# Kernel optimization log

Measured on AMD Instinct MI355X. Metric: run time of the kernel, lower is better.

Reference implementation:

```python
import jax, jax.numpy as jnp
import numpy as np

HEAD_DIM = 64
EPS = 1e-06


def yat_dense(x, kernel, bias):
    # YatDense (nmn): y = (x.W)^2 / (||x - w||^2 + eps) * alpha_scale + b
    dot = x @ kernel                                  # [..., F]
    x_sq = jnp.sum(x * x, axis=-1, keepdims=True)     # [..., 1]
    w_sq = jnp.sum(kernel * kernel, axis=0)           # [F]
    dist = x_sq + w_sq - 2.0 * dot                    # squared euclidean distance
    y = (dot * dot) / (dist + EPS)
    feats = kernel.shape[1]
    scale = np.sqrt(feats) / np.log1p(feats)          # alpha=1 scaling
    return y * jnp.asarray(scale, x.dtype) + bias


def apply_rope(q, k):
    # q,k: [B,H,T,D]; interleaved-pair rotation, base 10000 (dim=HEAD_DIM)
    B, H, T, D = q.shape
    half = D // 2
    pos = jnp.arange(T, dtype=jnp.float32)
    freqs = 10000.0 ** (-jnp.arange(half, dtype=jnp.float32) / half)
    ang = pos[:, None] * freqs[None, :]               # [T, half]
    sin = jnp.sin(ang)[None, None, :, :, None]        # [1,1,T,half,1]
    cos = jnp.cos(ang)[None, None, :, :, None]

    def rot(t):
        ts = t.reshape(B, H, T, half, 2)
        t0, t1 = ts[..., 0:1], ts[..., 1:2]
        out = jnp.concatenate([t0 * cos - t1 * sin, t1 * cos + t0 * sin], axis=-1)
        return out.reshape(B, H, T, D)

    return rot(q), rot(k)


def setup_inputs() -> dict:
    key = jax.random.key(0)
    B, T, C, H = 2, 2048, 1024, 16
    k1, k2, k3, k4, k5 = jax.random.split(key, 5)
    x = jax.random.normal(k1, (B, T, C), dtype=jnp.float32)
    # causal mask, broadcast over batch
    mask = jnp.broadcast_to(jnp.tril(jnp.ones((T, T), dtype=bool))[None], (B, T, T))
    s = 1.0 / np.sqrt(C)
    w_attn = jax.random.normal(k2, (C, 3 * C), dtype=jnp.float32) * s
    b_attn = jnp.zeros((3 * C,), dtype=jnp.float32)
    w_proj = jax.random.normal(k3, (C, C), dtype=jnp.float32) * s
    b_proj = jnp.zeros((C,), dtype=jnp.float32)
    return {"x": x, "mask": mask, "w_attn": w_attn, "b_attn": b_attn,
            "w_proj": w_proj, "b_proj": b_proj}


def reference(x, mask, w_attn, b_attn, w_proj, b_proj):
    B, T, C = x.shape
    H = C // HEAD_DIM
    qkv = yat_dense(x, w_attn, b_attn)                     # [B,T,3C]
    qkv = qkv.reshape(B, T, 3, H, HEAD_DIM)
    q, k, v = jnp.moveaxis(qkv, 2, 0)                      # each [B,T,H,hd]
    q = jnp.swapaxes(q, 1, 2)                              # [B,H,T,hd]
    k = jnp.swapaxes(k, 1, 2)
    v = jnp.swapaxes(v, 1, 2)
    q, k = apply_rope(q, k)
    scale = jnp.asarray(np.sqrt(HEAD_DIM), x.dtype)
    attn = jnp.einsum('bhqd,bhkd->bhqk', q, k) / scale     # [B,H,T,T]
    neg = jnp.finfo(x.dtype).min
    attn = jnp.where(mask[:, None, :, :], attn, neg)
    attn = jax.nn.softmax(attn, axis=-1)
    out = jnp.einsum('bhqk,bhkd->bhqd', attn, v)           # [B,H,T,hd]
    out = jnp.swapaxes(out, 1, 2).reshape(B, T, C)
    return yat_dense(out, w_proj, b_proj)
```

## Files before the change

kernel.cpp:

```cpp
#include <hip/hip_runtime.h>
#include <hip/hip_bf16.h>
#include <cmath>

#define BB 2
#define TT 2048
#define CC 1024
#define HH 16
#define DD 64
#define ROWS (BB*TT)
#define N1 (3*CC)
#define EPS 1e-6f

using short8 = __attribute__((ext_vector_type(8))) short;
using f32x4  = __attribute__((ext_vector_type(4))) float;

__device__ __forceinline__ void gl_lds16(const __hip_bfloat16* g, unsigned short* l) {
    __builtin_amdgcn_global_load_lds(
        (const __attribute__((address_space(1))) unsigned int*)(g),
        (__attribute__((address_space(3))) unsigned int*)(l), 16, 0, 0);
}

__device__ __forceinline__ unsigned int bf16pair(float a, float b) {
    __hip_bfloat16 ha = (__hip_bfloat16)a, hb = (__hip_bfloat16)b;
    unsigned short ua = *(unsigned short*)&ha, ub = *(unsigned short*)&hb;
    return (unsigned int)ua | ((unsigned int)ub << 16);
}

__device__ __forceinline__ float bf2f(unsigned short u) {
    unsigned int v = (unsigned int)u << 16;
    return *(float*)&v;
}

__global__ void aux_rowsq(const float* __restrict__ X, float* __restrict__ xsq,
                          __hip_bfloat16* __restrict__ Xb, float* __restrict__ osq,
                          float* __restrict__ rope,
                          float* __restrict__ wsqa, float* __restrict__ wsqp) {
    int blk = blockIdx.x;
    int t = threadIdx.x;
    if (blk >= ROWS) {
        int idx = (blk - ROWS) * 256 + t;
        if (idx < N1) wsqa[idx] = 0.f;
        if (idx < CC) wsqp[idx] = 0.f;
        if (idx < TT * 32) {
            int tt = idx >> 5, i = idx & 31;
            double freq = pow(10000.0, -(double)i / 32.0);
            float ang = (float)tt * (float)freq;
            rope[idx * 2 + 0] = cosf(ang);
            rope[idx * 2 + 1] = sinf(ang);
        }
        return;
    }
    int row = blk;
    const float* xr = X + (size_t)row * CC;
    __hip_bfloat16* br = Xb + (size_t)row * CC;
    float p = 0.f;
#pragma unroll
    for (int i = 0; i < 4; ++i) {
        float v = xr[t + i * 256];
        p += v * v;
        br[t + i * 256] = (__hip_bfloat16)v;
    }
#pragma unroll
    for (int off = 32; off > 0; off >>= 1) p += __shfl_xor(p, off, 64);
    __shared__ float s4[4];
    if ((t & 63) == 0) s4[t >> 6] = p;
    __syncthreads();
    if (t == 0) { xsq[row] = s4[0] + s4[1] + s4[2] + s4[3]; osq[row] = 0.f; }
}

__global__ void transpose2(const float* __restrict__ Wa, __hip_bfloat16* __restrict__ WaT,
                           float* __restrict__ wsqa,
                           const float* __restrict__ Wp, __hip_bfloat16* __restrict__ WpT,
                           float* __restrict__ wsqp) {
    const float* W; __hip_bfloat16* Wt; float* wsq; int N;
    if (blockIdx.z == 0) { W = Wa; Wt = WaT; wsq = wsqa; N = N1; }
    else { if (blockIdx.x >= 16) return; W = Wp; Wt = WpT; wsq = wsqp; N = CC; }
    const int K = CC;
    __shared__ unsigned short tile[64][65];
    int n0 = blockIdx.x * 64, k0 = blockIdx.y * 64;
    int c = threadIdx.x & 63, rg = threadIdx.x >> 6;
    float part = 0.f;
#pragma unroll
    for (int rr = 0; rr < 16; ++rr) {
        int r = rg + rr * 4;
        float f = W[(size_t)(k0 + r) * N + n0 + c];
        __hip_bfloat16 h = (__hip_bfloat16)f;
        tile[r][c] = *(unsigned short*)&h;
        part += f * f;
    }
    atomicAdd(&wsq[n0 + c], part);
    __syncthreads();
#pragma unroll
    for (int rr = 0; rr < 16; ++rr) {
        int r = rg + rr * 4;
        unsigned short u = tile[c][r];
        Wt[(size_t)(n0 + r) * K + k0 + c] = *(__hip_bfloat16*)&u;
    }
}

__global__ __launch_bounds__(256) void yat_gemm_qkv2(
    const __hip_bfloat16* __restrict__ A,
    const __hip_bfloat16* __restrict__ Bt,
    const float* __restrict__ xsq, const float* __restrict__ wsq,
    const float* __restrict__ bias,
    __hip_bfloat16* __restrict__ Qb, __hip_bfloat16* __restrict__ Kb,
    __hip_bfloat16* __restrict__ Vb, float scale) {
    const int K = CC;
    __shared__ __align__(16) unsigned short As0[128 * 32], As1[128 * 32];
    __shared__ __align__(16) unsigned short Bs0[128 * 32], Bs1[128 * 32];
    int tid = threadIdx.x;
    int wave = tid >> 6, lane = tid & 63, quad = lane >> 4, l16 = lane & 15;
    int wr = wave >> 1, wc = wave & 1;
    int m0 = blockIdx.y * 128, n0 = blockIdx.x * 128;

    f32x4 acc[4][4];
#pragma unroll
    for (int mt = 0; mt < 4; ++mt)
#pragma unroll
        for (int nt = 0; nt < 4; ++nt) acc[mt][nt] = f32x4{0.f, 0.f, 0.f, 0.f};

    int srow = lane >> 2, soff = (lane & 3) << 3;
    for (int k0 = 0; k0 < K; k0 += 64) {
        __syncthreads();
#pragma unroll
        for (int i = 0; i < 2; ++i) {
            int rowc = (wave * 2 + i) * 16;
            const __hip_bfloat16* ap = A + (size_t)(m0 + rowc + srow) * K + k0 + soff;
            gl_lds16(ap,      As0 + rowc * 32);
            gl_lds16(ap + 32, As1 + rowc * 32);
            const __hip_bfloat16* bp = Bt + (size_t)(n0 + rowc + srow) * K + k0 + soff;
            gl_lds16(bp,      Bs0 + rowc * 32);
            gl_lds16(bp + 32, Bs1 + rowc * 32);
        }
        __syncthreads();
#pragma unroll
        for (int h = 0; h < 2; ++h) {
            const unsigned short* Ah = h ? As1 : As0;
            const unsigned short* Bh = h ? Bs1 : Bs0;
            short8 af[4], bf[4];
#pragma unroll
            for (int mt = 0; mt < 4; ++mt)
                af[mt] = *(const short8*)(Ah + (wr * 64 + mt * 16 + l16) * 32 + quad * 8);
#pragma unroll
            for (int nt = 0; nt < 4; ++nt)
                bf[nt] = *(const short8*)(Bh + (wc * 64 + nt * 16 + l16) * 32 + quad * 8);
#pragma unroll
            for (int mt = 0; mt < 4; ++mt)
#pragma unroll
                for (int nt = 0; nt < 4; ++nt)
                    acc[mt][nt] = __builtin_amdgcn_mfma_f32_16x16x32_bf16(af[mt], bf[nt], acc[mt][nt], 0, 0, 0);
        }
    }
    int mb = m0 + wr * 64 + quad * 4;
#pragma unroll
    for (int nt = 0; nt < 4; ++nt) {
        int col = n0 + wc * 64 + nt * 16 + l16;
        float wq = wsq[col], bs = bias[col];
        int sec = col >> 10, cc2 = col & 1023;
        int h = cc2 >> 6, d = cc2 & 63;
        __hip_bfloat16* dst = (sec == 0) ? Qb : ((sec == 1) ? Kb : Vb);
#pragma unroll
        for (int mt = 0; mt < 4; ++mt) {
#pragma unroll
            for (int r = 0; r < 4; ++r) {
                int row = mb + mt * 16 + r;
                float dot = acc[mt][nt][r];
                float dist = xsq[row] + wq - 2.f * dot + EPS;
                float y = dot * dot / dist * scale + bs;
                int t = row & (TT - 1), bI = row >> 11;
                dst[(((size_t)bI * HH + h) * TT + t) * DD + d] = (__hip_bfloat16)y;
            }
        }
    }
}

__global__ __launch_bounds__(256) void ropek_vtrans(
    unsigned short* __restrict__ Kb, const unsigned short* __restrict__ Vb,
    __hip_bfloat16* __restrict__ Vtb, const float* __restrict__ rope) {
    int bh = blockIdx.y, t0 = blockIdx.x * 64, tid = threadIdx.x;
    __shared__ unsigned short vt[64][72];
    int r = tid >> 2, g = tid & 3;
    const unsigned short* src = Vb + ((size_t)bh * TT + t0 + r) * DD + g * 16;
    *(uint4*)&vt[r][g * 16]     = *(const uint4*)src;
    *(uint4*)&vt[r][g * 16 + 8] = *(const uint4*)(src + 8);
    {
        int t = t0 + r;
        unsigned short* kp = Kb + ((size_t)bh * TT + t) * DD + g * 16;
        union U8 { uint4 v; unsigned short s[8]; } k0v, k1v, o0, o1;
        k0v.v = *(const uint4*)kp;
        k1v.v = *(const uint4*)(kp + 8);
        const float* rp = rope + (size_t)t * 64 + g * 16;
#pragma unroll
        for (int u = 0; u < 8; ++u) {
            float c = rp[2 * u], sn = rp[2 * u + 1];
            unsigned short ev = (u < 4) ? k0v.s[2 * u]     : k1v.s[2 * u - 8];
            unsigned short ov = (u < 4) ? k0v.s[2 * u + 1] : k1v.s[2 * u - 7];
            float f0 = bf2f(ev), f1 = bf2f(ov);
            unsigned int pr = bf16pair(f0 * c - f1 * sn, f1 * c + f0 * sn);
            if (u < 4) ((unsigned int*)&o0)[u] = pr;
            else       ((unsigned int*)&o1)[u - 4] = pr;
        }
        *(uint4*)kp = o0.v;
        *(uint4*)(kp + 8) = o1.v;
    }
    __syncthreads();
    union U8b { uint4 v; unsigned short s[8]; };
#pragma unroll
    for (int p = 0; p < 2; ++p) {
        int d = (tid >> 3) + p * 32, tl = (tid & 7) * 8;
        U8b w;
#pragma unroll
        for (int j = 0; j < 8; ++j) w.s[j] = vt[tl + j][d];
        *(uint4*)(Vtb + ((size_t)bh * DD + d) * TT + t0 + tl) = w.v;
    }
}

__global__ __launch_bounds__(256, 3) void attn_mfma8(
    const __hip_bfloat16* __restrict__ Qb, const __hip_bfloat16* __restrict__ Kb,
    const __hip_bfloat16* __restrict__ Vtb, const float* __restrict__ rope,
    __hip_bfloat16* __restrict__ out, float* __restrict__ osq) {
    const float QSC = 0.125f * 1.44269504f;
    int i = blockIdx.x;
    int xcd = i & 7, jj = (i >> 3) & 3, s = i >> 5;
    int bh = xcd + 8 * jj;
    int b = bh >> 4, h = bh & 15;
    int tid = threadIdx.x;
    int wave = tid >> 6, lane = tid & 63, quad = lane >> 4, l16 = lane & 15;

    __shared__ __align__(16) unsigned short Ks[2][2][64 * 32];
    __shared__ __align__(16) unsigned short Vs[2][2][64 * 32];
    __shared__ __align__(16) unsigned short Ps[4][16 * 72];
    unsigned short* pp = &Ps[wave][0];

    const __hip_bfloat16* Qbase = Qb + (size_t)bh * TT * DD;
    const __hip_bfloat16* Kbase = Kb + (size_t)bh * TT * DD;
    const __hip_bfloat16* Vbase = Vtb + (size_t)bh * DD * TT;

    int srow = lane >> 2, soff = (lane & 3) * 8;
    short8 ones8;
#pragma unroll
    for (int u = 0; u < 8; ++u) ones8[u] = (short)0x3F80;

    int u0, u1, nunits;
    if (s < 8)       { u0 = s;      u1 = 15 - s; nunits = 2; }
    else if (s < 16) { u0 = s + 8;  u1 = 0;      nunits = 1; }
    else             { u0 = 47 - s; u1 = 0;      nunits = 1; }

    for (int un = 0; un < nunits; ++un) {
        int qblk = un ? u1 : u0;
        int qw = qblk * 64 + wave * 16;
        short8 qf0, qf1;
        {
            int t = qw + l16;
            const unsigned short* qr = (const unsigned short*)(Qbase + (size_t)t * DD) + quad * 8;
            union S8 { short8 v; unsigned short s[8]; } r0, r1, o0v, o1v;
            r0.v = *(const short8*)qr;
            r1.v = *(const short8*)(qr + 32);
            const float* rpa = rope + (size_t)t * 64 + quad * 8;
            const float* rpb = rpa + 32;
#pragma unroll
            for (int u = 0; u < 4; ++u) {
                float c = rpa[2 * u] * QSC, sn = rpa[2 * u + 1] * QSC;
                float e = bf2f(r0.s[2 * u]), o = bf2f(r0.s[2 * u + 1]);
                ((unsigned int*)&o0v)[u] = bf16pair(e * c - o * sn, o * c + e * sn);
                float c2 = rpb[2 * u] * QSC, sn2 = rpb[2 * u + 1] * QSC;
                float e2 = bf2f(r1.s[2 * u]), o2 = bf2f(r1.s[2 * u + 1]);
                ((unsigned int*)&o1v)[u] = bf16pair(e2 * c2 - o2 * sn2, o2 * c2 + e2 * sn2);
            }
            qf0 = o0v.v;
            qf1 = o1v.v;
        }
        f32x4 acc_o[4];
#pragma unroll
        for (int mt = 0; mt < 4; ++mt) acc_o[mt] = f32x4{0.f, 0.f, 0.f, 0.f};
        f32x4 acc_l = {0.f, 0.f, 0.f, 0.f};
        int q_g = qw + l16;

        __syncthreads();
        gl_lds16(Kbase + (size_t)(wave * 16 + srow) * DD + soff,      &Ks[0][0][wave * 512]);
        gl_lds16(Kbase + (size_t)(wave * 16 + srow) * DD + 32 + soff, &Ks[0][1][wave * 512]);
        gl_lds16(Vbase + (size_t)(wave * 16 + srow) * TT + soff,      &Vs[0][0][wave * 512]);
        gl_lds16(Vbase + (size_t)(wave * 16 + srow) * TT + 32 + soff, &Vs[0][1][wave * 512]);

        for (int kt = 0; kt <= qblk; ++kt) {
            int cur = kt & 1;
            int k0 = kt * 64;
            __syncthreads();
            if (kt < qblk) {
                int nb = cur ^ 1, kn = k0 + 64;
                gl_lds16(Kbase + (size_t)(kn + wave * 16 + srow) * DD + soff,      &Ks[nb][0][wave * 512]);
                gl_lds16(Kbase + (size_t)(kn + wave * 16 + srow) * DD + 32 + soff, &Ks[nb][1][wave * 512]);
                gl_lds16(Vbase + (size_t)(wave * 16 + srow) * TT + kn + soff,      &Vs[nb][0][wave * 512]);
                gl_lds16(Vbase + (size_t)(wave * 16 + srow) * TT + kn + 32 + soff, &Vs[nb][1][wave * 512]);
            }
            f32x4 accs[4];
#pragma unroll
            for (int mt = 0; mt < 4; ++mt) {
                short8 kf0 = *(const short8*)(&Ks[cur][0][(mt * 16 + l16) * 32 + quad * 8]);
                short8 kf1 = *(const short8*)(&Ks[cur][1][(mt * 16 + l16) * 32 + quad * 8]);
                f32x4 z = {0.f, 0.f, 0.f, 0.f};
                z = __builtin_amdgcn_mfma_f32_16x16x32_bf16(kf0, qf0, z, 0, 0, 0);
                accs[mt] = __builtin_amdgcn_mfma_f32_16x16x32_bf16(kf1, qf1, z, 0, 0, 0);
            }
            int limit = (kt == qblk) ? q_g : 0x7FFFFFFF;
#pragma unroll
            for (int mt = 0; mt < 4; ++mt) {
                int keyb = k0 + mt * 16 + quad * 4;
                float p0 = exp2f(accs[mt][0]);
                float p1 = exp2f(accs[mt][1]);
                float p2 = exp2f(accs[mt][2]);
                float p3 = exp2f(accs[mt][3]);
                p0 = (keyb + 0 <= limit) ? p0 : 0.f;
                p1 = (keyb + 1 <= limit) ? p1 : 0.f;
                p2 = (keyb + 2 <= limit) ? p2 : 0.f;
                p3 = (keyb + 3 <= limit) ? p3 : 0.f;
                uint2 w2;
                w2.x = bf16pair(p0, p1);
                w2.y = bf16pair(p2, p3);
                *(uint2*)(pp + l16 * 72 + mt * 16 + quad * 4) = w2;
            }
            short8 pf0 = *(const short8*)(pp + l16 * 72 + quad * 8);
            short8 pf1 = *(const short8*)(pp + l16 * 72 + 32 + quad * 8);
#pragma unroll
            for (int mt = 0; mt < 4; ++mt) {
                short8 vf0 = *(const short8*)(&Vs[cur][0][(mt * 16 + l16) * 32 + quad * 8]);
                short8 vf1 = *(const short8*)(&Vs[cur][1][(mt * 16 + l16) * 32 + quad * 8]);
                acc_o[mt] = __builtin_amdgcn_mfma_f32_16x16x32_bf16(vf0, pf0, acc_o[mt], 0, 0, 0);
                acc_o[mt] = __builtin_amdgcn_mfma_f32_16x16x32_bf16(vf1, pf1, acc_o[mt], 0, 0, 0);
            }
            acc_l = __builtin_amdgcn_mfma_f32_16x16x32_bf16(ones8, pf0, acc_l, 0, 0, 0);
            acc_l = __builtin_amdgcn_mfma_f32_16x16x32_bf16(ones8, pf1, acc_l, 0, 0, 0);
        }
        float inv = 1.f / acc_l[0];
        float part = 0.f;
#pragma unroll
        for (int mt = 0; mt < 4; ++mt) {
            float o0 = acc_o[mt][0] * inv;
            float o1 = acc_o[mt][1] * inv;
            float o2 = acc_o[mt][2] * inv;
            float o3 = acc_o[mt][3] * inv;
            part += o0 * o0 + o1 * o1 + o2 * o2 + o3 * o3;
            uint2 w2;
            w2.x = bf16pair(o0, o1);
            w2.y = bf16pair(o2, o3);
            *(uint2*)(pp + l16 * 72 + mt * 16 + quad * 4) = w2;
        }
        part += __shfl_xor(part, 16, 64);
        part += __shfl_xor(part, 32, 64);
        if (quad == 0) atomicAdd(&osq[(size_t)b * TT + qw + l16], part);
        int rw = lane >> 2, cg = lane & 3;
        uint4 o0 = *(const uint4*)(pp + rw * 72 + cg * 16);
        uint4 o1 = *(const uint4*)(pp + rw * 72 + cg * 16 + 8);
        __hip_bfloat16* orow = out + (size_t)(b * TT + qw + rw) * CC + h * DD + cg * 16;
        *(uint4*)(orow) = o0;
        *(uint4*)(orow + 8) = o1;
    }
}

template<int TM, int TN, typename OutT>
__global__ __launch_bounds__(256) void yat_gemm_bk64(
    const __hip_bfloat16* __restrict__ A,
    const __hip_bfloat16* __restrict__ Bt,
    const float* __restrict__ xsq, const float* __restrict__ wsq,
    const float* __restrict__ bias, OutT* __restrict__ C,
    int M, int N, int K, float scale) {
    constexpr int MT = TM / 32;
    constexpr int NT = TN / 32;
    constexpr int IA = TM / 64;
    constexpr int IB = TN / 64;
    __shared__ __align__(16) unsigned short As0[TM * 32];
    __shared__ __align__(16) unsigned short As1[TM * 32];
    __shared__ __align__(16) unsigned short Bs0[TN * 32];
    __shared__ __align__(16) unsigned short Bs1[TN * 32];
    int tid = threadIdx.x;
    int wave = tid >> 6, lane = tid & 63, quad = lane >> 4, l16 = lane & 15;
    int wr = wave >> 1, wc = wave & 1;
    int m0 = blockIdx.y * TM, n0 = blockIdx.x * TN;

    f32x4 acc[MT][NT];
#pragma unroll
    for (int mt = 0; mt < MT; ++mt)
#pragma unroll
        for (int nt = 0; nt < NT; ++nt) acc[mt][nt] = f32x4{0.f, 0.f, 0.f, 0.f};

    int srow = lane >> 2, soff = (lane & 3) << 3;
    for (int k0 = 0; k0 < K; k0 += 64) {
        __syncthreads();
#pragma unroll
        for (int i = 0; i < IA; ++i) {
            int rowc = (wave * IA + i) * 16;
            const __hip_bfloat16* ap = A + (size_t)(m0 + rowc + srow) * K + k0 + soff;
            gl_lds16(ap,      As0 + rowc * 32);
            gl_lds16(ap + 32, As1 + rowc * 32);
        }
#pragma unroll
        for (int i = 0; i < IB; ++i) {
            int rowc = (wave * IB + i) * 16;
            const __hip_bfloat16* bp = Bt + (size_t)(n0 + rowc + srow) * K + k0 + soff;
            gl_lds16(bp,      Bs0 + rowc * 32);
            gl_lds16(bp + 32, Bs1 + rowc * 32);
        }
        __syncthreads();
#pragma unroll
        for (int h = 0; h < 2; ++h) {
            const unsigned short* Ah = h ? As1 : As0;
            const unsigned short* Bh = h ? Bs1 : Bs0;
            short8 af[MT], bf[NT];
#pragma unroll
            for (int mt = 0; mt < MT; ++mt)
                af[mt] = *(const short8*)(Ah + (wr * (TM / 2) + mt * 16 + l16) * 32 + quad * 8);
#pragma unroll
            for (int nt = 0; nt < NT; ++nt)
                bf[nt] = *(const short8*)(Bh + (wc * (TN / 2) + nt * 16 + l16) * 32 + quad * 8);
#pragma unroll
            for (int mt = 0; mt < MT; ++mt)
#pragma unroll
                for (int nt = 0; nt < NT; ++nt)
                    acc[mt][nt] = __builtin_amdgcn_mfma_f32_16x16x32_bf16(af[mt], bf[nt], acc[mt][nt], 0, 0, 0);
        }
    }
    int mb = m0 + wr * (TM / 2) + quad * 4;
#pragma unroll
    for (int nt = 0; nt < NT; ++nt) {
        int col = n0 + wc * (TN / 2) + nt * 16 + l16;
        float wq = wsq[col];
        float bs = bias[col];
#pragma unroll
        for (int mt = 0; mt < MT; ++mt) {
#pragma unroll
            for (int r = 0; r < 4; ++r) {
                int row = mb + mt * 16 + r;
                float dot = acc[mt][nt][r];
                float dist = xsq[row] + wq - 2.f * dot + EPS;
                C[(size_t)row * N + col] = (OutT)(dot * dot / dist * scale + bs);
            }
        }
    }
}

extern "C" void kernel_launch(void* const* d_in, const int* in_sizes, int n_in,
                              void* d_out, int out_size, void* d_ws, size_t ws_size,
                              hipStream_t stream) {
    const float* x      = (const float*)d_in[0];
    const float* w_attn = (const float*)d_in[2];
    const float* b_attn = (const float*)d_in[3];
    const float* w_proj = (const float*)d_in[4];
    const float* b_proj = (const float*)d_in[5];
    float* out = (float*)d_out;

    char* ws = (char*)d_ws;
    __hip_bfloat16* xbf  = (__hip_bfloat16*)(ws + 0);
    __hip_bfloat16* aout = (__hip_bfloat16*)(ws + 8388608);
    __hip_bfloat16* watT = (__hip_bfloat16*)(ws + 16777216);
    __hip_bfloat16* wpT  = (__hip_bfloat16*)(ws + 23068672);
    float*          rope = (float*)(ws + 25165824);
    float*          xsq  = (float*)(ws + 25690112);
    float*          osq  = (float*)(ws + 25706496);
    float*          wsqa = (float*)(ws + 25722880);
    float*          wsqp = (float*)(ws + 25735168);
    __hip_bfloat16* Qb   = (__hip_bfloat16*)(ws + 25739264);
    __hip_bfloat16* Kb   = (__hip_bfloat16*)(ws + 34127872);
    __hip_bfloat16* Vb   = (__hip_bfloat16*)(ws + 42516480);
    __hip_bfloat16* Vtb  = (__hip_bfloat16*)(ws + 50905088);

    float scale1 = (float)(sqrt(3072.0) / log1p(3072.0));
    float scale2 = (float)(sqrt(1024.0) / log1p(1024.0));

    aux_rowsq<<<ROWS + 256, 256, 0, stream>>>(x, xsq, xbf, osq, rope, wsqa, wsqp);
    transpose2<<<dim3(48, 16, 2), 256, 0, stream>>>(w_attn, watT, wsqa, w_proj, wpT, wsqp);
    yat_gemm_qkv2<<<dim3(N1 / 128, ROWS / 128), 256, 0, stream>>>(
        xbf, watT, xsq, wsqa, b_attn, Qb, Kb, Vb, scale1);
    ropek_vtrans<<<dim3(TT / 64, BB * HH), 256, 0, stream>>>(
        (unsigned short*)Kb, (const unsigned short*)Vb, Vtb, rope);
    attn_mfma8<<<768, 256, 0, stream>>>(Qb, Kb, Vtb, rope, aout, osq);
    yat_gemm_bk64<64, 64, float><<<dim3(CC / 64, ROWS / 64), 256, 0, stream>>>(
        aout, wpT, osq, wsqp, b_proj, out, ROWS, CC, CC, scale2);
}
```

Baseline: 220.6 us.

## Fuse prep kernels, use one query block per attention workgroup with register P shuffle

Weight transposes and squared-norm computation move into the prep kernel. Each block now owns a whole 64-column strip, which removes the atomics and one launch, but only 64 blocks remain for that work. The attention kernel now runs one query block per workgroup across 1024 blocks, raising launch bounds to occupancy 4. It passes the P tile to the PV MFMA through cross-lane shuffles instead of an LDS round trip, and reuses the K buffer for output staging. The risks are causal imbalance across blocks and the low parallelism of the 64 transpose blocks.

```diff
diff --git a/kernel.cpp b/kernel.cpp
--- a/kernel.cpp
+++ b/kernel.cpp
@@ -31,16 +31,36 @@
     return *(float*)&v;
 }
 
-__global__ void aux_rowsq(const float* __restrict__ X, float* __restrict__ xsq,
-                          __hip_bfloat16* __restrict__ Xb, float* __restrict__ osq,
-                          float* __restrict__ rope,
-                          float* __restrict__ wsqa, float* __restrict__ wsqp) {
+__global__ void prep_all(const float* __restrict__ X, float* __restrict__ xsq,
+                         __hip_bfloat16* __restrict__ Xb, float* __restrict__ osq,
+                         float* __restrict__ rope,
+                         const float* __restrict__ Wa, __hip_bfloat16* __restrict__ WaT,
+                         float* __restrict__ wsqa,
+                         const float* __restrict__ Wp, __hip_bfloat16* __restrict__ WpT,
+                         float* __restrict__ wsqp) {
     int blk = blockIdx.x;
     int t = threadIdx.x;
-    if (blk >= ROWS) {
+    if (blk < ROWS) {
+        int row = blk;
+        const float* xr = X + (size_t)row * CC;
+        __hip_bfloat16* br = Xb + (size_t)row * CC;
+        float p = 0.f;
+#pragma unroll
+        for (int i = 0; i < 4; ++i) {
+            float v = xr[t + i * 256];
+            p += v * v;
+            br[t + i * 256] = (__hip_bfloat16)v;
+        }
+#pragma unroll
+        for (int off = 32; off > 0; off >>= 1) p += __shfl_xor(p, off, 64);
+        __shared__ float s4[4];
+        if ((t & 63) == 0) s4[t >> 6] = p;
+        __syncthreads();
+        if (t == 0) { xsq[row] = s4[0] + s4[1] + s4[2] + s4[3]; osq[row] = 0.f; }
+        return;
+    }
+    if (blk < ROWS + 256) {
         int idx = (blk - ROWS) * 256 + t;
-        if (idx < N1) wsqa[idx] = 0.f;
-        if (idx < CC) wsqp[idx] = 0.f;
         if (idx < TT * 32) {
             int tt = idx >> 5, i = idx & 31;
             double freq = pow(10000.0, -(double)i / 32.0);
@@ -50,52 +70,36 @@
         }
         return;
     }
-    int row = blk;
-    const float* xr = X + (size_t)row * CC;
-    __hip_bfloat16* br = Xb + (size_t)row * CC;
-    float p = 0.f;
-#pragma unroll
-    for (int i = 0; i < 4; ++i) {
-        float v = xr[t + i * 256];
-        p += v * v;
-        br[t + i * 256] = (__hip_bfloat16)v;
-    }
-#pragma unroll
-    for (int off = 32; off > 0; off >>= 1) p += __shfl_xor(p, off, 64);
-    __shared__ float s4[4];
-    if ((t & 63) == 0) s4[t >> 6] = p;
+    int strip = blk - (ROWS + 256);
+    const float* W; __hip_bfloat16* Wt; float* wsq; int N, n0;
+    if (strip < 48) { W = Wa; Wt = WaT; wsq = wsqa; N = N1; n0 = strip * 64; }
+    else            { W = Wp; Wt = WpT; wsq = wsqp; N = CC; n0 = (strip - 48) * 64; }
+    __shared__ unsigned short tile[64][65];
+    __shared__ float sred[4][64];
+    int c = t & 63, rg = t >> 6;
+    float part = 0.f;
+    for (int kt = 0; kt < 16; ++kt) {
+        int k0 = kt * 64;
+        __syncthreads();
+#pragma unroll
+        for (int rr = 0; rr < 16; ++rr) {
+            int r = rg + rr * 4;
+            float f = W[(size_t)(k0 + r) * N + n0 + c];
+            __hip_bfloat16 hh = (__hip_bfloat16)f;
+            tile[r][c] = *(unsigned short*)&hh;
+            part += f * f;
+        }
+        __syncthreads();
+#pragma unroll
+        for (int rr = 0; rr < 16; ++rr) {
+            int r = rg + rr * 4;
+            unsigned short u = tile[c][r];
+            Wt[(size_t)(n0 + r) * CC + k0 + c] = *(__hip_bfloat16*)&u;
+        }
+    }
+    sred[rg][c] = part;
     __syncthreads();
-    if (t == 0) { xsq[row] = s4[0] + s4[1] + s4[2] + s4[3]; osq[row] = 0.f; }
-}
-
-__global__ void transpose2(const float* __restrict__ Wa, __hip_bfloat16* __restrict__ WaT,
-                           float* __restrict__ wsqa,
-                           const float* __restrict__ Wp, __hip_bfloat16* __restrict__ WpT,
-                           float* __restrict__ wsqp) {
-    const float* W; __hip_bfloat16* Wt; float* wsq; int N;
-    if (blockIdx.z == 0) { W = Wa; Wt = WaT; wsq = wsqa; N = N1; }
-    else { if (blockIdx.x >= 16) return; W = Wp; Wt = WpT; wsq = wsqp; N = CC; }
-    const int K = CC;
-    __shared__ unsigned short tile[64][65];
-    int n0 = blockIdx.x * 64, k0 = blockIdx.y * 64;
-    int c = threadIdx.x & 63, rg = threadIdx.x >> 6;
-    float part = 0.f;
-#pragma unroll
-    for (int rr = 0; rr < 16; ++rr) {
-        int r = rg + rr * 4;
-        float f = W[(size_t)(k0 + r) * N + n0 + c];
-        __hip_bfloat16 h = (__hip_bfloat16)f;
-        tile[r][c] = *(unsigned short*)&h;
-        part += f * f;
-    }
-    atomicAdd(&wsq[n0 + c], part);
-    __syncthreads();
-#pragma unroll
-    for (int rr = 0; rr < 16; ++rr) {
-        int r = rg + rr * 4;
-        unsigned short u = tile[c][r];
-        Wt[(size_t)(n0 + r) * K + k0 + c] = *(__hip_bfloat16*)&u;
-    }
+    if (rg == 0) wsq[n0 + c] = sred[0][c] + sred[1][c] + sred[2][c] + sred[3][c];
 }
 
 __global__ __launch_bounds__(256) void yat_gemm_qkv2(
@@ -215,146 +219,158 @@
     }
 }
 
-__global__ __launch_bounds__(256, 3) void attn_mfma8(
+__global__ __launch_bounds__(256, 4) void attn_mfma9(
     const __hip_bfloat16* __restrict__ Qb, const __hip_bfloat16* __restrict__ Kb,
     const __hip_bfloat16* __restrict__ Vtb, const float* __restrict__ rope,
     __hip_bfloat16* __restrict__ out, float* __restrict__ osq) {
     const float QSC = 0.125f * 1.44269504f;
     int i = blockIdx.x;
-    int xcd = i & 7, jj = (i >> 3) & 3, s = i >> 5;
-    int bh = xcd + 8 * jj;
+    int xcd = i & 7;
+    int r0 = i >> 3;
+    int bh = xcd + 8 * (r0 & 3);
+    int rr = r0 >> 2;
+    int v = rr & 7, s2 = rr >> 3;
+    int qblk = (s2 == 0) ? v : (s2 == 1) ? (15 - v) : (s2 == 2) ? (16 + v) : (31 - v);
     int b = bh >> 4, h = bh & 15;
     int tid = threadIdx.x;
     int wave = tid >> 6, lane = tid & 63, quad = lane >> 4, l16 = lane & 15;
 
     __shared__ __align__(16) unsigned short Ks[2][2][64 * 32];
     __shared__ __align__(16) unsigned short Vs[2][2][64 * 32];
-    __shared__ __align__(16) unsigned short Ps[4][16 * 72];
-    unsigned short* pp = &Ps[wave][0];
 
     const __hip_bfloat16* Qbase = Qb + (size_t)bh * TT * DD;
     const __hip_bfloat16* Kbase = Kb + (size_t)bh * TT * DD;
     const __hip_bfloat16* Vbase = Vtb + (size_t)bh * DD * TT;
 
+    int qw = qblk * 64 + wave * 16;
+    short8 qf0, qf1;
+    {
+        int t = qw + l16;
+        const unsigned short* qr = (const unsigned short*)(Qbase + (size_t)t * DD) + quad * 8;
+        union S8 { short8 v; unsigned short s[8]; } r0v, r1v, o0v, o1v;
+        r0v.v = *(const short8*)qr;
+        r1v.v = *(const short8*)(qr + 32);
+        const float* rpa = rope + (size_t)t * 64 + quad * 8;
+        const float* rpb = rpa + 32;
+#pragma unroll
+        for (int u = 0; u < 4; ++u) {
+            float c = rpa[2 * u] * QSC, sn = rpa[2 * u + 1] * QSC;
+            float e = bf2f(r0v.s[2 * u]), o = bf2f(r0v.s[2 * u + 1]);
+            ((unsigned int*)&o0v)[u] = bf16pair(e * c - o * sn, o * c + e * sn);
+            float c2 = rpb[2 * u] * QSC, sn2 = rpb[2 * u + 1] * QSC;
+            float e2 = bf2f(r1v.s[2 * u]), o2 = bf2f(r1v.s[2 * u + 1]);
+            ((unsigned int*)&o1v)[u] = bf16pair(e2 * c2 - o2 * sn2, o2 * c2 + e2 * sn2);
+        }
+        qf0 = o0v.v;
+        qf1 = o1v.v;
+    }
+    short8 ones8;
+#pragma unroll
+    for (int u = 0; u < 8; ++u) ones8[u] = (short)0x3F80;
+
+    f32x4 acc_o[4];
+#pragma unroll
+    for (int mt = 0; mt < 4; ++mt) acc_o[mt] = f32x4{0.f, 0.f, 0.f, 0.f};
+    f32x4 acc_l = {0.f, 0.f, 0.f, 0.f};
+
     int srow = lane >> 2, soff = (lane & 3) * 8;
-    short8 ones8;
-#pragma unroll
-    for (int u = 0; u < 8; ++u) ones8[u] = (short)0x3F80;
-
-    int u0, u1, nunits;
-    if (s < 8)       { u0 = s;      u1 = 15 - s; nunits = 2; }
-    else if (s < 16) { u0 = s + 8;  u1 = 0;      nunits = 1; }
-    else             { u0 = 47 - s; u1 = 0;      nunits = 1; }
-
-    for (int un = 0; un < nunits; ++un) {
-        int qblk = un ? u1 : u0;
-        int qw = qblk * 64 + wave * 16;
-        short8 qf0, qf1;
+    int q_g = qw + l16;
+    int src0 = l16 + (quad & 1) * 32;
+    int src1 = src0 + 16;
+    bool lowq = quad < 2;
+
+    gl_lds16(Kbase + (size_t)(wave * 16 + srow) * DD + soff,      &Ks[0][0][wave * 512]);
+    gl_lds16(Kbase + (size_t)(wave * 16 + srow) * DD + 32 + soff, &Ks[0][1][wave * 512]);
+    gl_lds16(Vbase + (size_t)(wave * 16 + srow) * TT + soff,      &Vs[0][0][wave * 512]);
+    gl_lds16(Vbase + (size_t)(wave * 16 + srow) * TT + 32 + soff, &Vs[0][1][wave * 512]);
+
+    for (int kt = 0; kt <= qblk; ++kt) {
+        int cur = kt & 1;
+        int k0 = kt * 64;
+        __syncthreads();
+        if (kt < qblk) {
+            int nb = cur ^ 1, kn = k0 + 64;
+            gl_lds16(Kbase + (size_t)(kn + wave * 16 + srow) * DD + soff,      &Ks[nb][0][wave * 512]);
+            gl_lds16(Kbase + (size_t)(kn + wave * 16 + srow) * DD + 32 + soff, &Ks[nb][1][wave * 512]);
+            gl_lds16(Vbase + (size_t)(wave * 16 + srow) * TT + kn + soff,      &Vs[nb][0][wave * 512]);
+            gl_lds16(Vbase + (size_t)(wave * 16 + srow) * TT + kn + 32 + soff, &Vs[nb][1][wave * 512]);
+        }
+        f32x4 accs[4];
+#pragma unroll
+        for (int mt = 0; mt < 4; ++mt) {
+            short8 kf0 = *(const short8*)(&Ks[cur][0][(mt * 16 + l16) * 32 + quad * 8]);
+            short8 kf1 = *(const short8*)(&Ks[cur][1][(mt * 16 + l16) * 32 + quad * 8]);
+            f32x4 z = {0.f, 0.f, 0.f, 0.f};
+            z = __builtin_amdgcn_mfma_f32_16x16x32_bf16(kf0, qf0, z, 0, 0, 0);
+            accs[mt] = __builtin_amdgcn_mfma_f32_16x16x32_bf16(kf1, qf1, z, 0, 0, 0);
+        }
+        int limit = (kt == qblk) ? q_g : 0x7FFFFFFF;
+        unsigned int pk[4][2];
+#pragma unroll
+        for (int mt = 0; mt < 4; ++mt) {
+            int keyb = k0 + mt * 16 + quad * 4;
+            float p0 = exp2f(accs[mt][0]);
+            float p1 = exp2f(accs[mt][1]);
+            float p2 = exp2f(accs[mt][2]);
+            float p3 = exp2f(accs[mt][3]);
+            p0 = (keyb + 0 <= limit) ? p0 : 0.f;
+            p1 = (keyb + 1 <= limit) ? p1 : 0.f;
+            p2 = (keyb + 2 <= limit) ? p2 : 0.f;
+            p3 = (keyb + 3 <= limit) ? p3 : 0.f;
+            pk[mt][0] = bf16pair(p0, p1);
+            pk[mt][1] = bf16pair(p2, p3);
+        }
+        union PF { uint4 u; short8 v; } pf0u, pf1u;
         {
-            int t = qw + l16;
-            const unsigned short* qr = (const unsigned short*)(Qbase + (size_t)t * DD) + quad * 8;
-            union S8 { short8 v; unsigned short s[8]; } r0, r1, o0v, o1v;
-            r0.v = *(const short8*)qr;
-            r1.v = *(const short8*)(qr + 32);
-            const float* rpa = rope + (size_t)t * 64 + quad * 8;
-            const float* rpb = rpa + 32;
-#pragma unroll
-            for (int u = 0; u < 4; ++u) {
-                float c = rpa[2 * u] * QSC, sn = rpa[2 * u + 1] * QSC;
-                float e = bf2f(r0.s[2 * u]), o = bf2f(r0.s[2 * u + 1]);
-                ((unsigned int*)&o0v)[u] = bf16pair(e * c - o * sn, o * c + e * sn);
-                float c2 = rpb[2 * u] * QSC, sn2 = rpb[2 * u + 1] * QSC;
-                float e2 = bf2f(r1.s[2 * u]), o2 = bf2f(r1.s[2 * u + 1]);
-                ((unsigned int*)&o1v)[u] = bf16pair(e2 * c2 - o2 * sn2, o2 * c2 + e2 * sn2);
-            }
-            qf0 = o0v.v;
-            qf1 = o1v.v;
-        }
-        f32x4 acc_o[4];
-#pragma unroll
-        for (int mt = 0; mt < 4; ++mt) acc_o[mt] = f32x4{0.f, 0.f, 0.f, 0.f};
-        f32x4 acc_l = {0.f, 0.f, 0.f, 0.f};
-        int q_g = qw + l16;
-
-        __syncthreads();
-        gl_lds16(Kbase + (size_t)(wave * 16 + srow) * DD + soff,      &Ks[0][0][wave * 512]);
-        gl_lds16(Kbase + (size_t)(wave * 16 + srow) * DD + 32 + soff, &Ks[0][1][wave * 512]);
-        gl_lds16(Vbase + (size_t)(wave * 16 + srow) * TT + soff,      &Vs[0][0][wave * 512]);
-        gl_lds16(Vbase + (size_t)(wave * 16 + srow) * TT + 32 + soff, &Vs[0][1][wave * 512]);
-
-        for (int kt = 0; kt <= qblk; ++kt) {
-            int cur = kt & 1;
-            int k0 = kt * 64;
-            __syncthreads();
-            if (kt < qblk) {
-                int nb = cur ^ 1, kn = k0 + 64;
-                gl_lds16(Kbase + (size_t)(kn + wave * 16 + srow) * DD + soff,      &Ks[nb][0][wave * 512]);
-                gl_lds16(Kbase + (size_t)(kn + wave * 16 + srow) * DD + 32 + soff, &Ks[nb][1][wave * 512]);
-                gl_lds16(Vbase + (size_t)(wave * 16 + srow) * TT + kn + soff,      &Vs[nb][0][wave * 512]);
-                gl_lds16(Vbase + (size_t)(wave * 16 + srow) * TT + kn + 32 + soff, &Vs[nb][1][wave * 512]);
-            }
-            f32x4 accs[4];
-#pragma unroll
-            for (int mt = 0; mt < 4; ++mt) {
-                short8 kf0 = *(const short8*)(&Ks[cur][0][(mt * 16 + l16) * 32 + quad * 8]);
-                short8 kf1 = *(const short8*)(&Ks[cur][1][(mt * 16 + l16) * 32 + quad * 8]);
-                f32x4 z = {0.f, 0.f, 0.f, 0.f};
-                z = __builtin_amdgcn_mfma_f32_16x16x32_bf16(kf0, qf0, z, 0, 0, 0);
-                accs[mt] = __builtin_amdgcn_mfma_f32_16x16x32_bf16(kf1, qf1, z, 0, 0, 0);
-            }
-            int limit = (kt == qblk) ? q_g : 0x7FFFFFFF;
-#pragma unroll
-            for (int mt = 0; mt < 4; ++mt) {
-                int keyb = k0 + mt * 16 + quad * 4;
-                float p0 = exp2f(accs[mt][0]);
-                float p1 = exp2f(accs[mt][1]);
-                float p2 = exp2f(accs[mt][2]);
-                float p3 = exp2f(accs[mt][3]);
-                p0 = (keyb + 0 <= limit) ? p0 : 0.f;
-                p1 = (keyb + 1 <= limit) ? p1 : 0.f;
-                p2 = (keyb + 2 <= limit) ? p2 : 0.f;
-                p3 = (keyb + 3 <= limit) ? p3 : 0.f;
-                uint2 w2;
-                w2.x = bf16pair(p0, p1);
-                w2.y = bf16pair(p2, p3);
-                *(uint2*)(pp + l16 * 72 + mt * 16 + quad * 4) = w2;
-            }
-            short8 pf0 = *(const short8*)(pp + l16 * 72 + quad * 8);
-            short8 pf1 = *(const short8*)(pp + l16 * 72 + 32 + quad * 8);
-#pragma unroll
-            for (int mt = 0; mt < 4; ++mt) {
-                short8 vf0 = *(const short8*)(&Vs[cur][0][(mt * 16 + l16) * 32 + quad * 8]);
-                short8 vf1 = *(const short8*)(&Vs[cur][1][(mt * 16 + l16) * 32 + quad * 8]);
-                acc_o[mt] = __builtin_amdgcn_mfma_f32_16x16x32_bf16(vf0, pf0, acc_o[mt], 0, 0, 0);
-                acc_o[mt] = __builtin_amdgcn_mfma_f32_16x16x32_bf16(vf1, pf1, acc_o[mt], 0, 0, 0);
-            }
-            acc_l = __builtin_amdgcn_mfma_f32_16x16x32_bf16(ones8, pf0, acc_l, 0, 0, 0);
-            acc_l = __builtin_amdgcn_mfma_f32_16x16x32_bf16(ones8, pf1, acc_l, 0, 0, 0);
-        }
-        float inv = 1.f / acc_l[0];
-        float part = 0.f;
+            int a0 = __shfl((int)pk[0][0], src0, 64), a1 = __shfl((int)pk[0][1], src0, 64);
+            int a2 = __shfl((int)pk[0][0], src1, 64), a3 = __shfl((int)pk[0][1], src1, 64);
+            int b0 = __shfl((int)pk[1][0], src0, 64), b1 = __shfl((int)pk[1][1], src0, 64);
+            int b2 = __shfl((int)pk[1][0], src1, 64), b3 = __shfl((int)pk[1][1], src1, 64);
+            pf0u.u = lowq ? uint4{(unsigned)a0, (unsigned)a1, (unsigned)a2, (unsigned)a3}
+                          : uint4{(unsigned)b0, (unsigned)b1, (unsigned)b2, (unsigned)b3};
+            int c0 = __shfl((int)pk[2][0], src0, 64), c1 = __shfl((int)pk[2][1], src0, 64);
+            int c2 = __shfl((int)pk[2][0], src1, 64), c3 = __shfl((int)pk[2][1], src1, 64);
+            int d0 = __shfl((int)pk[3][0], src0, 64), d1 = __shfl((int)pk[3][1], src0, 64);
+            int d2 = __shfl((int)pk[3][0], src1, 64), d3 = __shfl((int)pk[3][1], src1, 64);
+            pf1u.u = lowq ? uint4{(unsigned)c0, (unsigned)c1, (unsigned)c2, (unsigned)c3}
+                          : uint4{(unsigned)d0, (unsigned)d1, (unsigned)d2, (unsigned)d3};
+        }
+        short8 pf0 = pf0u.v, pf1 = pf1u.v;
 #pragma unroll
         for (int mt = 0; mt < 4; ++mt) {
-            float o0 = acc_o[mt][0] * inv;
-            float o1 = acc_o[mt][1] * inv;
-            float o2 = acc_o[mt][2] * inv;
-            float o3 = acc_o[mt][3] * inv;
-            part += o0 * o0 + o1 * o1 + o2 * o2 + o3 * o3;
-            uint2 w2;
-            w2.x = bf16pair(o0, o1);
-            w2.y = bf16pair(o2, o3);
-            *(uint2*)(pp + l16 * 72 + mt * 16 + quad * 4) = w2;
-        }
-        part += __shfl_xor(part, 16, 64);
-        part += __shfl_xor(part, 32, 64);
-        if (quad == 0) atomicAdd(&osq[(size_t)b * TT + qw + l16], part);
-        int rw = lane >> 2, cg = lane & 3;
-        uint4 o0 = *(const uint4*)(pp + rw * 72 + cg * 16);
-        uint4 o1 = *(const uint4*)(pp + rw * 72 + cg * 16 + 8);
-        __hip_bfloat16* orow = out + (size_t)(b * TT + qw + rw) * CC + h * DD + cg * 16;
-        *(uint4*)(orow) = o0;
-        *(uint4*)(orow + 8) = o1;
-    }
+            short8 vf0 = *(const short8*)(&Vs[cur][0][(mt * 16 + l16) * 32 + quad * 8]);
+            short8 vf1 = *(const short8*)(&Vs[cur][1][(mt * 16 + l16) * 32 + quad * 8]);
+            acc_o[mt] = __builtin_amdgcn_mfma_f32_16x16x32_bf16(vf0, pf0, acc_o[mt], 0, 0, 0);
+            acc_o[mt] = __builtin_amdgcn_mfma_f32_16x16x32_bf16(vf1, pf1, acc_o[mt], 0, 0, 0);
+        }
+        acc_l = __builtin_amdgcn_mfma_f32_16x16x32_bf16(ones8, pf0, acc_l, 0, 0, 0);
+        acc_l = __builtin_amdgcn_mfma_f32_16x16x32_bf16(ones8, pf1, acc_l, 0, 0, 0);
+    }
+    __syncthreads();
+    unsigned short* pp = (unsigned short*)Ks + wave * 1152;
+    float inv = 1.f / acc_l[0];
+    float part = 0.f;
+#pragma unroll
+    for (int mt = 0; mt < 4; ++mt) {
+        float o0 = acc_o[mt][0] * inv;
+        float o1 = acc_o[mt][1] * inv;
+        float o2 = acc_o[mt][2] * inv;
+        float o3 = acc_o[mt][3] * inv;
+        part += o0 * o0 + o1 * o1 + o2 * o2 + o3 * o3;
+        uint2 w2;
+        w2.x = bf16pair(o0, o1);
+        w2.y = bf16pair(o2, o3);
+        *(uint2*)(pp + l16 * 72 + mt * 16 + quad * 4) = w2;
+    }
+    part += __shfl_xor(part, 16, 64);
+    part += __shfl_xor(part, 32, 64);
+    if (quad == 0) atomicAdd(&osq[(size_t)b * TT + qw + l16], part);
+    int rw = lane >> 2, cg = lane & 3;
+    uint4 o0 = *(const uint4*)(pp + rw * 72 + cg * 16);
+    uint4 o1 = *(const uint4*)(pp + rw * 72 + cg * 16 + 8);
+    __hip_bfloat16* orow = out + (size_t)(b * TT + qw + rw) * CC + h * DD + cg * 16;
+    *(uint4*)(orow) = o0;
+    *(uint4*)(orow + 8) = o1;
 }
 
 template<int TM, int TN, typename OutT>
@@ -466,13 +482,13 @@
     float scale1 = (float)(sqrt(3072.0) / log1p(3072.0));
     float scale2 = (float)(sqrt(1024.0) / log1p(1024.0));
 
-    aux_rowsq<<<ROWS + 256, 256, 0, stream>>>(x, xsq, xbf, osq, rope, wsqa, wsqp);
-    transpose2<<<dim3(48, 16, 2), 256, 0, stream>>>(w_attn, watT, wsqa, w_proj, wpT, wsqp);
+    prep_all<<<ROWS + 256 + 64, 256, 0, stream>>>(
+        x, xsq, xbf, osq, rope, w_attn, watT, wsqa, w_proj, wpT, wsqp);
     yat_gemm_qkv2<<<dim3(N1 / 128, ROWS / 128), 256, 0, stream>>>(
         xbf, watT, xsq, wsqa, b_attn, Qb, Kb, Vb, scale1);
     ropek_vtrans<<<dim3(TT / 64, BB * HH), 256, 0, stream>>>(
         (unsigned short*)Kb, (const unsigned short*)Vb, Vtb, rope);
-    attn_mfma8<<<768, 256, 0, stream>>>(Qb, Kb, Vtb, rope, aout, osq);
+    attn_mfma9<<<1024, 256, 0, stream>>>(Qb, Kb, Vtb, rope, aout, osq);
     yat_gemm_bk64<64, 64, float><<<dim3(CC / 64, ROWS / 64), 256, 0, stream>>>(
         aout, wpT, osq, wsqp, b_proj, out, ROWS, CC, CC, scale2);
 }
```

New measurement: 232.7 us. 1.06x slower.
